# Kernel optimization log

Measured on AMD Instinct MI355X. Metric: run time of the kernel, lower is better.

## Reference

```python
import jax, jax.numpy as jnp
import numpy as np
import math

B, S, HID, NH = 2, 2048, 1024, 16
HD = HID // NH  # head_dim = 64
TEMPERATURE = 1.0


def setup_inputs() -> dict:
    key = jax.random.key(0)
    ks = jax.random.split(key, 6)
    w = lambda k: (jax.random.normal(k, (HID, HID), dtype=jnp.float32) * 0.02)
    return {
        "hidden_states": jax.random.normal(ks[0], (B, S, HID), dtype=jnp.float32),
        "attention_mask": jnp.ones((B, S), dtype=jnp.float32),
        "Wq": w(ks[1]), "bq": jnp.zeros((HID,), jnp.float32),
        "Wk": w(ks[2]), "bk": jnp.zeros((HID,), jnp.float32),
        "Wv": w(ks[3]), "bv": jnp.zeros((HID,), jnp.float32),
        "Wo": w(ks[4]), "bo": jnp.zeros((HID,), jnp.float32),
    }


def reference(hidden_states, attention_mask, Wq, bq, Wk, bk, Wv, bv, Wo, bo):
    b, s, hid = hidden_states.shape
    heads = lambda x: x.reshape(b, s, NH, HD).transpose(0, 2, 1, 3)  # [b,h,s,d]

    q = heads(hidden_states @ Wq.T + bq)
    k = heads(hidden_states @ Wk.T + bk)
    v = heads(hidden_states @ Wv.T + bv)

    # padding mask applied multiplicatively to k and v
    m = attention_mask[:, None, :, None]  # [b,1,s,1]
    k = k * m
    v = v * m

    # auxiliary Hopfield state: k^T @ v per head -> [b,h,d,d]
    state = jnp.einsum("bhsd,bhse->bhde", k, v)

    # energy / scores
    energy = jnp.einsum("bhqd,bhkd->bhqk", q, k) / (TEMPERATURE * math.sqrt(HD))
    causal = jnp.triu(jnp.ones((s, s), dtype=bool), k=1)  # True above diagonal
    energy = jnp.where(causal[None, None], -jnp.inf, energy)
    energy = jnp.where(attention_mask[:, None, None, :] == 0, -jnp.inf, energy)

    attn = jax.nn.softmax(energy, axis=-1)
    out = jnp.einsum("bhqk,bhkd->bhqd", attn, v)
    out = out.transpose(0, 2, 1, 3).reshape(b, s, hid)
    out = out @ Wo.T + bo
    return out, state
```

## Files before the change

kernel.cpp:

```cpp
#include <hip/hip_runtime.h>
#include <hip/hip_bf16.h>

#define B_ 2
#define S_ 2048
#define HID_ 1024
#define NH_ 16
#define HD_ 64
#define MTOK (B_*S_)
#define LDQKV 3072

typedef __attribute__((ext_vector_type(8))) __bf16 bf16x8;
typedef __attribute__((ext_vector_type(4))) __bf16 bf16x4;
typedef __attribute__((ext_vector_type(4))) float f32x4;

__device__ __forceinline__ void gl16(__bf16* lds, const __bf16* g) {
  __builtin_amdgcn_global_load_lds(
      (const __attribute__((address_space(1))) void*)g,
      (__attribute__((address_space(3))) void*)lds, 16, 0, 0);
}
__device__ __forceinline__ void gl4(float* lds, const float* g) {
  __builtin_amdgcn_global_load_lds(
      (const __attribute__((address_space(1))) void*)g,
      (__attribute__((address_space(3))) void*)lds, 4, 0, 0);
}

__global__ __launch_bounds__(256) void cast_all(
    const float* __restrict__ X,
    const float* __restrict__ Wq, const float* __restrict__ Wk,
    const float* __restrict__ Wv, const float* __restrict__ Wo,
    __bf16* __restrict__ Xb, __bf16* __restrict__ Wqkvb, __bf16* __restrict__ Wob)
{
  int i = blockIdx.x * 256 + threadIdx.x;
  const float* src; __bf16* dst; int j;
  if (i < (1 << 20))              { src = X;  dst = Xb;                 j = i; }
  else if (i < (1<<20)+(1<<18))   { src = Wq; dst = Wqkvb;              j = i - (1<<20); }
  else if (i < (1<<20)+(2<<18))   { src = Wk; dst = Wqkvb + (1<<20);    j = i - (1<<20) - (1<<18); }
  else if (i < (1<<20)+(3<<18))   { src = Wv; dst = Wqkvb + (2<<20);    j = i - (1<<20) - (2<<18); }
  else                            { src = Wo; dst = Wob;                j = i - (1<<20) - (3<<18); }
  float4 v = reinterpret_cast<const float4*>(src)[j];
  bf16x4 o;
  o[0] = (__bf16)v.x; o[1] = (__bf16)v.y; o[2] = (__bf16)v.z; o[3] = (__bf16)v.w;
  reinterpret_cast<bf16x4*>(dst)[j] = o;
}

__global__ __launch_bounds__(256) void gemm_qkv(
    const __bf16* __restrict__ A, const __bf16* __restrict__ W,
    const float* __restrict__ bq, const float* __restrict__ bk,
    const float* __restrict__ bv, const float* __restrict__ mask,
    __bf16* __restrict__ C)
{
  __shared__ __bf16 As[128 * 32];
  __shared__ __bf16 Bs[128 * 32];
  const int t = threadIdx.x;
  const int m0 = blockIdx.y * 128;
  const int n0 = blockIdx.x * 128;
  const int lane = t & 63;
  const int w = t >> 6;
  const int wr = (w >> 1) * 64;
  const int wc = (w & 1) * 64;
  const int fr = lane & 15;
  const int kg = lane >> 4;

  f32x4 acc[4][4];
  #pragma unroll
  for (int i = 0; i < 4; i++)
    #pragma unroll
    for (int j = 0; j < 4; j++) acc[i][j] = (f32x4)0.f;

  const int srow = w * 16 + (lane >> 2);
  const int scol = (lane & 3) * 8;
  const __bf16* ap0 = A + (size_t)(m0 + srow) * HID_ + scol;
  const __bf16* ap1 = A + (size_t)(m0 + 64 + srow) * HID_ + scol;
  const __bf16* wp0 = W + (size_t)(n0 + srow) * HID_ + scol;
  const __bf16* wp1 = W + (size_t)(n0 + 64 + srow) * HID_ + scol;

  for (int k0 = 0; k0 < HID_; k0 += 32) {
    __syncthreads();
    gl16(&As[w * 512], ap0 + k0);
    gl16(&As[2048 + w * 512], ap1 + k0);
    gl16(&Bs[w * 512], wp0 + k0);
    gl16(&Bs[2048 + w * 512], wp1 + k0);
    __syncthreads();
    bf16x8 af[4], bf[4];
    #pragma unroll
    for (int m = 0; m < 4; m++) af[m] = *(const bf16x8*)&As[(wr + m*16 + fr) * 32 + kg*8];
    #pragma unroll
    for (int n = 0; n < 4; n++) bf[n] = *(const bf16x8*)&Bs[(wc + n*16 + fr) * 32 + kg*8];
    #pragma unroll
    for (int m = 0; m < 4; m++)
      #pragma unroll
      for (int n = 0; n < 4; n++)
        acc[m][n] = __builtin_amdgcn_mfma_f32_16x16x32_bf16(af[m], bf[n], acc[m][n], 0, 0, 0);
  }

  const int region = n0 >> 10;
  const float* bias = region == 0 ? bq : (region == 1 ? bk : bv);
  const int nloc = n0 & 1023;

  #pragma unroll
  for (int m = 0; m < 4; m++) {
    #pragma unroll
    for (int r = 0; r < 4; r++) {
      int row = m0 + wr + m*16 + kg*4 + r;
      float rs = region ? mask[row] : 1.f;
      #pragma unroll
      for (int n = 0; n < 4; n++) {
        int c = wc + n*16 + fr;
        float v = (acc[m][n][r] + bias[nloc + c]) * rs;
        C[(size_t)row * LDQKV + n0 + c] = (__bf16)v;
      }
    }
  }
}

__global__ __launch_bounds__(256) void gemm_o(
    const __bf16* __restrict__ A, const __bf16* __restrict__ W,
    const float* __restrict__ bias, float* __restrict__ C)
{
  __shared__ __bf16 As[128 * 32];
  __shared__ __bf16 Bs[128 * 32];
  const int t = threadIdx.x;
  const int m0 = blockIdx.y * 128;
  const int n0 = blockIdx.x * 128;
  const int lane = t & 63;
  const int w = t >> 6;
  const int wr = (w >> 1) * 64;
  const int wc = (w & 1) * 64;
  const int fr = lane & 15;
  const int kg = lane >> 4;

  f32x4 acc[4][4];
  #pragma unroll
  for (int i = 0; i < 4; i++)
    #pragma unroll
    for (int j = 0; j < 4; j++) acc[i][j] = (f32x4)0.f;

  const int srow = w * 16 + (lane >> 2);
  const int scol = (lane & 3) * 8;
  const __bf16* ap0 = A + (size_t)(m0 + srow) * HID_ + scol;
  const __bf16* ap1 = A + (size_t)(m0 + 64 + srow) * HID_ + scol;
  const __bf16* wp0 = W + (size_t)(n0 + srow) * HID_ + scol;
  const __bf16* wp1 = W + (size_t)(n0 + 64 + srow) * HID_ + scol;

  for (int k0 = 0; k0 < HID_; k0 += 32) {
    __syncthreads();
    gl16(&As[w * 512], ap0 + k0);
    gl16(&As[2048 + w * 512], ap1 + k0);
    gl16(&Bs[w * 512], wp0 + k0);
    gl16(&Bs[2048 + w * 512], wp1 + k0);
    __syncthreads();
    bf16x8 af[4], bf[4];
    #pragma unroll
    for (int m = 0; m < 4; m++) af[m] = *(const bf16x8*)&As[(wr + m*16 + fr) * 32 + kg*8];
    #pragma unroll
    for (int n = 0; n < 4; n++) bf[n] = *(const bf16x8*)&Bs[(wc + n*16 + fr) * 32 + kg*8];
    #pragma unroll
    for (int m = 0; m < 4; m++)
      #pragma unroll
      for (int n = 0; n < 4; n++)
        acc[m][n] = __builtin_amdgcn_mfma_f32_16x16x32_bf16(af[m], bf[n], acc[m][n], 0, 0, 0);
  }

  #pragma unroll
  for (int m = 0; m < 4; m++) {
    #pragma unroll
    for (int r = 0; r < 4; r++) {
      int row = m0 + wr + m*16 + kg*4 + r;
      #pragma unroll
      for (int n = 0; n < 4; n++) {
        int col = n0 + wc + n*16 + fr;
        C[(size_t)row * HID_ + col] = acc[m][n][r] + bias[col];
      }
    }
  }
}

__global__ __launch_bounds__(256) void transpose_bf16(
    const __bf16* __restrict__ in, int ldin, __bf16* __restrict__ out)
{
  __shared__ __bf16 tile[64][68];
  const int tok0 = blockIdx.x * 64;
  const int f0 = blockIdx.y * 64;
  const int t = threadIdx.x;
  const int r = t >> 2;
  const int c0 = (t & 3) * 16;
  const __bf16* src = in + (size_t)(tok0 + r) * ldin + f0 + c0;
  *(bf16x8*)&tile[r][c0]     = *(const bf16x8*)src;
  *(bf16x8*)&tile[r][c0 + 8] = *(const bf16x8*)(src + 8);
  __syncthreads();
  bf16x8 o0, o1;
  #pragma unroll
  for (int j = 0; j < 8; j++) { o0[j] = tile[c0 + j][r]; o1[j] = tile[c0 + 8 + j][r]; }
  __bf16* dst = out + (size_t)(f0 + r) * MTOK + tok0 + c0;
  *(bf16x8*)dst = o0;
  *(bf16x8*)(dst + 8) = o1;
}

#define SCALE_LOG2E 0.18033688011112043f

__device__ __forceinline__ bf16x8 ld_swz(const __bf16* base, int row, int xb) {
  return *(const bf16x8*)((const char*)base + row * 128 + (xb ^ ((row & 7) << 4)));
}
__device__ __forceinline__ void st_swz16(__bf16* base, int row, int colbyte, __bf16 v) {
  *(__bf16*)((char*)base + row * 128 + (colbyte ^ ((row & 7) << 4))) = v;
}
__device__ __forceinline__ bf16x8 ld_swz256(const __bf16* base, int row, int xb) {
  return *(const bf16x8*)((const char*)base + row * 256 + (xb ^ ((row & 7) << 4)));
}

__global__ __launch_bounds__(512) void flash_mfma(
    const __bf16* __restrict__ Q, const __bf16* __restrict__ K,
    const __bf16* __restrict__ Vt, const float* __restrict__ mask,
    __bf16* __restrict__ O)
{
  __shared__ __bf16 Ks[2][64 * 64];
  __shared__ __bf16 Vs[2][64 * 64];
  __shared__ __bf16 Ps[8][16 * 64];
  __shared__ float mk[2][64];

  const int bh = blockIdx.x;
  const int qt = (int)(gridDim.y - 1) - (int)blockIdx.y;
  const int b = bh >> 4, h = bh & 15;
  const int t = threadIdx.x;
  const int w = t >> 6;
  const int lane = t & 63;
  const int fc = lane & 15;
  const int kg = lane >> 4;
  const int g4 = kg * 4;

  const int q0w = qt * 128 + w * 16;
  const size_t tokbase = (size_t)b * S_;

  const int rr = lane >> 3;
  const int cswz = ((lane & 7) ^ rr) * 8;
  const int ktmax = 2 * qt + 1;

  gl16(&Ks[0][w * 512], K + (tokbase + (size_t)(w * 8 + rr)) * LDQKV + h * HD_ + cswz);
  gl16(&Vs[0][w * 512], Vt + (size_t)(h * HD_ + w * 8 + rr) * MTOK + tokbase + cswz);
  gl4(&mk[0][0], mask + tokbase + lane);

  bf16x8 qa[2];
  {
    const __bf16* qp = Q + (tokbase + q0w + fc) * LDQKV + h * HD_;
    qa[0] = *(const bf16x8*)(qp + kg * 8);
    qa[1] = *(const bf16x8*)(qp + 32 + kg * 8);
  }

  bf16x8 ones;
  #pragma unroll
  for (int j = 0; j < 8; j++) ones[j] = (__bf16)1.f;

  f32x4 acc[4], accl;
  #pragma unroll
  for (int n = 0; n < 4; n++) acc[n] = (f32x4)0.f;
  accl = (f32x4)0.f;

  __bf16* pw = &Ps[w][0];

  for (int kt = 0; kt <= ktmax; ++kt) {
    const int cur = kt & 1;
    if (kt < ktmax) {
      const int nxt = cur ^ 1;
      gl16(&Ks[nxt][w * 512],
           K + (tokbase + (size_t)((kt + 1) * 64 + w * 8 + rr)) * LDQKV + h * HD_ + cswz);
      gl16(&Vs[nxt][w * 512],
           Vt + (size_t)(h * HD_ + w * 8 + rr) * MTOK + tokbase + (kt + 1) * 64 + cswz);
      gl4(&mk[nxt][0], mask + tokbase + (kt + 1) * 64 + lane);
      asm volatile("s_waitcnt vmcnt(3)" ::: "memory");
    } else {
      asm volatile("s_waitcnt vmcnt(0)" ::: "memory");
    }
    __builtin_amdgcn_sched_barrier(0);
    __builtin_amdgcn_s_barrier();

    if (kt * 64 <= q0w + 15) {
      const __bf16* ks = &Ks[cur][0];
      const __bf16* vs = &Vs[cur][0];
      f32x4 s[4];
      #pragma unroll
      for (int n = 0; n < 4; n++) s[n] = (f32x4)0.f;
      #pragma unroll
      for (int kd = 0; kd < 2; kd++)
        #pragma unroll
        for (int n = 0; n < 4; n++) {
          bf16x8 kf = ld_swz(ks, n * 16 + fc, kd * 64 + kg * 16);
          s[n] = __builtin_amdgcn_mfma_f32_16x16x32_bf16(qa[kd], kf, s[n], 0, 0, 0);
        }

      bool okm[4];
      #pragma unroll
      for (int n = 0; n < 4; n++) okm[n] = (mk[cur][n * 16 + fc] != 0.f);

      const bool fullt = (kt * 64 + 63 <= q0w);
      if (fullt) {
        #pragma unroll
        for (int r = 0; r < 4; r++)
          #pragma unroll
          for (int n = 0; n < 4; n++) {
            float p = okm[n] ? exp2f(s[n][r] * SCALE_LOG2E) : 0.f;
            st_swz16(pw, g4 + r, (n * 16 + fc) * 2, (__bf16)p);
          }
      } else {
        #pragma unroll
        for (int r = 0; r < 4; r++) {
          const int qg = q0w + g4 + r;
          #pragma unroll
          for (int n = 0; n < 4; n++) {
            bool ok = okm[n] && (kt * 64 + n * 16 + fc <= qg);
            float p = ok ? exp2f(s[n][r] * SCALE_LOG2E) : 0.f;
            st_swz16(pw, g4 + r, (n * 16 + fc) * 2, (__bf16)p);
          }
        }
      }

      #pragma unroll
      for (int kc = 0; kc < 2; kc++) {
        bf16x8 pf = ld_swz(pw, fc, kc * 64 + kg * 16);
        accl = __builtin_amdgcn_mfma_f32_16x16x32_bf16(pf, ones, accl, 0, 0, 0);
        #pragma unroll
        for (int n = 0; n < 4; n++) {
          bf16x8 vf = ld_swz(vs, n * 16 + fc, kc * 64 + kg * 16);
          acc[n] = __builtin_amdgcn_mfma_f32_16x16x32_bf16(pf, vf, acc[n], 0, 0, 0);
        }
      }
    }
    __builtin_amdgcn_s_barrier();
  }

  #pragma unroll
  for (int r = 0; r < 4; r++) {
    float inv = accl[r] > 0.f ? 1.f / accl[r] : 0.f;
    __bf16* op = O + (tokbase + q0w + g4 + r) * HID_ + h * HD_;
    #pragma unroll
    for (int n = 0; n < 4; n++)
      op[n * 16 + fc] = (__bf16)(acc[n][r] * inv);
  }
}

__global__ __launch_bounds__(256) void state_mfma(
    const __bf16* __restrict__ Kt, const __bf16* __restrict__ Vt,
    float* __restrict__ part)
{
  __shared__ __bf16 Kl[64 * 128];
  __shared__ __bf16 Vl[64 * 128];
  const int bh = blockIdx.x, sc = blockIdx.y;
  const int b = bh >> 4, h = bh & 15;
  const int t = threadIdx.x;
  const int w = t >> 6;
  const int lane = t & 63;
  const int fc = lane & 15;
  const int kg = lane >> 4;
  const size_t colbase = (size_t)b * S_ + sc * 128;
  const int rloc = lane >> 4;
  const int cb = (lane & 15) * 16;

  #pragma unroll
  for (int c = 0; c < 4; c++) {
    int row = w * 16 + c * 4 + rloc;
    int scol = (cb ^ ((row & 7) << 4)) >> 1;
    gl16(&Kl[(w * 16 + c * 4) * 128], Kt + (size_t)(h * HD_ + row) * MTOK + colbase + scol);
    gl16(&Vl[(w * 16 + c * 4) * 128], Vt + (size_t)(h * HD_ + row) * MTOK + colbase + scol);
  }
  __syncthreads();

  f32x4 acc[4];
  #pragma unroll
  for (int n = 0; n < 4; n++) acc[n] = (f32x4)0.f;
  #pragma unroll
  for (int ks = 0; ks < 4; ks++) {
    bf16x8 af = ld_swz256(Kl, w * 16 + fc, ks * 64 + kg * 16);
    #pragma unroll
    for (int n = 0; n < 4; n++) {
      bf16x8 bfr = ld_swz256(Vl, n * 16 + fc, ks * 64 + kg * 16);
      acc[n] = __builtin_amdgcn_mfma_f32_16x16x32_bf16(af, bfr, acc[n], 0, 0, 0);
    }
  }

  float* dst = part + (((size_t)bh * 16 + sc) << 12);
  #pragma unroll
  for (int n = 0; n < 4; n++)
    #pragma unroll
    for (int r = 0; r < 4; r++)
      dst[(w * 16 + kg * 4 + r) * 64 + n * 16 + fc] = acc[n][r];
}

__global__ __launch_bounds__(256) void state_reduce(
    const float* __restrict__ part, float* __restrict__ out)
{
  int i = blockIdx.x * 256 + threadIdx.x;
  int bh = i >> 12, de = i & 4095;
  float s = 0.f;
  #pragma unroll
  for (int sc = 0; sc < 16; sc++) s += part[(((size_t)bh * 16 + sc) << 12) + de];
  out[i] = s;
}

extern "C" void kernel_launch(void* const* d_in, const int* in_sizes, int n_in,
                              void* d_out, int out_size, void* d_ws, size_t ws_size,
                              hipStream_t stream)
{
  const float* hs   = (const float*)d_in[0];
  const float* mask = (const float*)d_in[1];
  const float* Wq   = (const float*)d_in[2];
  const float* bq   = (const float*)d_in[3];
  const float* Wk   = (const float*)d_in[4];
  const float* bk   = (const float*)d_in[5];
  const float* Wv   = (const float*)d_in[6];
  const float* bv   = (const float*)d_in[7];
  const float* Wo   = (const float*)d_in[8];
  const float* bo   = (const float*)d_in[9];
  float* out = (float*)d_out;

  char* ws = (char*)d_ws;
  __bf16* Wqkvb = (__bf16*)(ws);
  __bf16* Wob   = (__bf16*)(ws + (6u  << 20));
  __bf16* Xb    = (__bf16*)(ws + (8u  << 20));
  __bf16* QKV   = (__bf16*)(ws + (16u << 20));
  __bf16* Ob    = (__bf16*)(ws + (40u << 20));
  float*  part  = (float*)(ws + (48u << 20));

  cast_all<<<8192, 256, 0, stream>>>(hs, Wq, Wk, Wv, Wo, Xb, Wqkvb, Wob);

  gemm_qkv<<<dim3(LDQKV / 128, MTOK / 128), 256, 0, stream>>>(
      Xb, Wqkvb, bq, bk, bv, mask, QKV);

  __bf16* Vtg = Xb;
  transpose_bf16<<<dim3(MTOK / 64, HID_ / 64), 256, 0, stream>>>(QKV + 2048, LDQKV, Vtg);

  flash_mfma<<<dim3(B_ * NH_, S_ / 128), 512, 0, stream>>>(
      QKV, QKV + 1024, Vtg, mask, Ob);

  gemm_o<<<dim3(HID_ / 128, MTOK / 128), 256, 0, stream>>>(Ob, Wob, bo, out);

  __bf16* Ktg = Wqkvb;
  transpose_bf16<<<dim3(MTOK / 64, HID_ / 64), 256, 0, stream>>>(QKV + 1024, LDQKV, Ktg);

  state_mfma<<<dim3(B_ * NH_, 16), 256, 0, stream>>>(Ktg, Vtg, part);
  state_reduce<<<512, 256, 0, stream>>>(part, out + (size_t)MTOK * HID_);
}
```

Baseline: 144.1 us.

## Pair causal query tiles per block and merge K/V transposes into one launch

The flash attention kernel now has each block handle two query tiles, y and 15-y. The causal work per block is therefore balanced, and each K/V tile loaded into shared memory serves both query tiles, while the grid is halved to 8 tiles per head. The separate K and V transpose kernels are merged into a single launch with a z dimension. Buffers are remapped so the state partials reuse the Ob region after gemm_o. The cost is more registers per thread (two accumulator sets), which may lower occupancy, and fewer blocks overall.

```diff
diff --git a/kernel.cpp b/kernel.cpp
--- a/kernel.cpp
+++ b/kernel.cpp
@@ -175,16 +175,19 @@
   }
 }
 
-__global__ __launch_bounds__(256) void transpose_bf16(
-    const __bf16* __restrict__ in, int ldin, __bf16* __restrict__ out)
+__global__ __launch_bounds__(256) void transpose_kv(
+    const __bf16* __restrict__ Kin, const __bf16* __restrict__ Vin,
+    __bf16* __restrict__ Kt, __bf16* __restrict__ Vt)
 {
   __shared__ __bf16 tile[64][68];
   const int tok0 = blockIdx.x * 64;
   const int f0 = blockIdx.y * 64;
+  const __bf16* in = blockIdx.z ? Vin : Kin;
+  __bf16* out = blockIdx.z ? Vt : Kt;
   const int t = threadIdx.x;
   const int r = t >> 2;
   const int c0 = (t & 3) * 16;
-  const __bf16* src = in + (size_t)(tok0 + r) * ldin + f0 + c0;
+  const __bf16* src = in + (size_t)(tok0 + r) * LDQKV + f0 + c0;
   *(bf16x8*)&tile[r][c0]     = *(const bf16x8*)src;
   *(bf16x8*)&tile[r][c0 + 8] = *(const bf16x8*)(src + 8);
   __syncthreads();
@@ -208,6 +211,58 @@
   return *(const bf16x8*)((const char*)base + row * 256 + (xb ^ ((row & 7) << 4)));
 }
 
+__device__ __forceinline__ void attn_tile(
+    const __bf16* __restrict__ ks, const __bf16* __restrict__ vs,
+    const bool (&okm)[4], __bf16* __restrict__ pw,
+    const bf16x8 (&qa)[2], f32x4 (&acc)[4], f32x4& accl,
+    const bf16x8 ones, int q0w, int kt, int fc, int kg)
+{
+  f32x4 s[4];
+  #pragma unroll
+  for (int n = 0; n < 4; n++) s[n] = (f32x4)0.f;
+  #pragma unroll
+  for (int kd = 0; kd < 2; kd++)
+    #pragma unroll
+    for (int n = 0; n < 4; n++) {
+      bf16x8 kf = ld_swz(ks, n * 16 + fc, kd * 64 + kg * 16);
+      s[n] = __builtin_amdgcn_mfma_f32_16x16x32_bf16(qa[kd], kf, s[n], 0, 0, 0);
+    }
+
+  const int g4 = kg * 4;
+  const bool fullt = (kt * 64 + 63 <= q0w);
+  if (fullt) {
+    #pragma unroll
+    for (int r = 0; r < 4; r++)
+      #pragma unroll
+      for (int n = 0; n < 4; n++) {
+        float p = okm[n] ? exp2f(s[n][r] * SCALE_LOG2E) : 0.f;
+        st_swz16(pw, g4 + r, (n * 16 + fc) * 2, (__bf16)p);
+      }
+  } else {
+    #pragma unroll
+    for (int r = 0; r < 4; r++) {
+      const int qg = q0w + g4 + r;
+      #pragma unroll
+      for (int n = 0; n < 4; n++) {
+        bool ok = okm[n] && (kt * 64 + n * 16 + fc <= qg);
+        float p = ok ? exp2f(s[n][r] * SCALE_LOG2E) : 0.f;
+        st_swz16(pw, g4 + r, (n * 16 + fc) * 2, (__bf16)p);
+      }
+    }
+  }
+
+  #pragma unroll
+  for (int kc = 0; kc < 2; kc++) {
+    bf16x8 pf = ld_swz(pw, fc, kc * 64 + kg * 16);
+    accl = __builtin_amdgcn_mfma_f32_16x16x32_bf16(pf, ones, accl, 0, 0, 0);
+    #pragma unroll
+    for (int n = 0; n < 4; n++) {
+      bf16x8 vf = ld_swz(vs, n * 16 + fc, kc * 64 + kg * 16);
+      acc[n] = __builtin_amdgcn_mfma_f32_16x16x32_bf16(pf, vf, acc[n], 0, 0, 0);
+    }
+  }
+}
+
 __global__ __launch_bounds__(512) void flash_mfma(
     const __bf16* __restrict__ Q, const __bf16* __restrict__ K,
     const __bf16* __restrict__ Vt, const float* __restrict__ mask,
@@ -215,11 +270,12 @@
 {
   __shared__ __bf16 Ks[2][64 * 64];
   __shared__ __bf16 Vs[2][64 * 64];
-  __shared__ __bf16 Ps[8][16 * 64];
+  __shared__ __bf16 Ps[8][2][16 * 64];
   __shared__ float mk[2][64];
 
   const int bh = blockIdx.x;
-  const int qt = (int)(gridDim.y - 1) - (int)blockIdx.y;
+  const int y = blockIdx.y;
+  const int qtA = y, qtB = 15 - y;
   const int b = bh >> 4, h = bh & 15;
   const int t = threadIdx.x;
   const int w = t >> 6;
@@ -228,34 +284,39 @@
   const int kg = lane >> 4;
   const int g4 = kg * 4;
 
-  const int q0w = qt * 128 + w * 16;
+  const int q0A = qtA * 128 + w * 16;
+  const int q0B = qtB * 128 + w * 16;
   const size_t tokbase = (size_t)b * S_;
 
   const int rr = lane >> 3;
   const int cswz = ((lane & 7) ^ rr) * 8;
-  const int ktmax = 2 * qt + 1;
+  const int ktmax = 2 * qtB + 1;
 
   gl16(&Ks[0][w * 512], K + (tokbase + (size_t)(w * 8 + rr)) * LDQKV + h * HD_ + cswz);
   gl16(&Vs[0][w * 512], Vt + (size_t)(h * HD_ + w * 8 + rr) * MTOK + tokbase + cswz);
   gl4(&mk[0][0], mask + tokbase + lane);
 
-  bf16x8 qa[2];
+  bf16x8 qaA[2], qaB[2];
   {
-    const __bf16* qp = Q + (tokbase + q0w + fc) * LDQKV + h * HD_;
-    qa[0] = *(const bf16x8*)(qp + kg * 8);
-    qa[1] = *(const bf16x8*)(qp + 32 + kg * 8);
+    const __bf16* qp = Q + (tokbase + q0A + fc) * LDQKV + h * HD_;
+    qaA[0] = *(const bf16x8*)(qp + kg * 8);
+    qaA[1] = *(const bf16x8*)(qp + 32 + kg * 8);
+    const __bf16* qp2 = Q + (tokbase + q0B + fc) * LDQKV + h * HD_;
+    qaB[0] = *(const bf16x8*)(qp2 + kg * 8);
+    qaB[1] = *(const bf16x8*)(qp2 + 32 + kg * 8);
   }
 
   bf16x8 ones;
   #pragma unroll
   for (int j = 0; j < 8; j++) ones[j] = (__bf16)1.f;
 
-  f32x4 acc[4], accl;
-  #pragma unroll
-  for (int n = 0; n < 4; n++) acc[n] = (f32x4)0.f;
-  accl = (f32x4)0.f;
-
-  __bf16* pw = &Ps[w][0];
+  f32x4 accA[4], acclA, accB[4], acclB;
+  #pragma unroll
+  for (int n = 0; n < 4; n++) { accA[n] = (f32x4)0.f; accB[n] = (f32x4)0.f; }
+  acclA = (f32x4)0.f; acclB = (f32x4)0.f;
+
+  __bf16* pwA = &Ps[w][0][0];
+  __bf16* pwB = &Ps[w][1][0];
 
   for (int kt = 0; kt <= ktmax; ++kt) {
     const int cur = kt & 1;
@@ -273,67 +334,28 @@
     __builtin_amdgcn_sched_barrier(0);
     __builtin_amdgcn_s_barrier();
 
-    if (kt * 64 <= q0w + 15) {
-      const __bf16* ks = &Ks[cur][0];
-      const __bf16* vs = &Vs[cur][0];
-      f32x4 s[4];
-      #pragma unroll
-      for (int n = 0; n < 4; n++) s[n] = (f32x4)0.f;
-      #pragma unroll
-      for (int kd = 0; kd < 2; kd++)
-        #pragma unroll
-        for (int n = 0; n < 4; n++) {
-          bf16x8 kf = ld_swz(ks, n * 16 + fc, kd * 64 + kg * 16);
-          s[n] = __builtin_amdgcn_mfma_f32_16x16x32_bf16(qa[kd], kf, s[n], 0, 0, 0);
-        }
-
-      bool okm[4];
-      #pragma unroll
-      for (int n = 0; n < 4; n++) okm[n] = (mk[cur][n * 16 + fc] != 0.f);
-
-      const bool fullt = (kt * 64 + 63 <= q0w);
-      if (fullt) {
-        #pragma unroll
-        for (int r = 0; r < 4; r++)
-          #pragma unroll
-          for (int n = 0; n < 4; n++) {
-            float p = okm[n] ? exp2f(s[n][r] * SCALE_LOG2E) : 0.f;
-            st_swz16(pw, g4 + r, (n * 16 + fc) * 2, (__bf16)p);
-          }
-      } else {
-        #pragma unroll
-        for (int r = 0; r < 4; r++) {
-          const int qg = q0w + g4 + r;
-          #pragma unroll
-          for (int n = 0; n < 4; n++) {
-            bool ok = okm[n] && (kt * 64 + n * 16 + fc <= qg);
-            float p = ok ? exp2f(s[n][r] * SCALE_LOG2E) : 0.f;
-            st_swz16(pw, g4 + r, (n * 16 + fc) * 2, (__bf16)p);
-          }
-        }
-      }
-
-      #pragma unroll
-      for (int kc = 0; kc < 2; kc++) {
-        bf16x8 pf = ld_swz(pw, fc, kc * 64 + kg * 16);
-        accl = __builtin_amdgcn_mfma_f32_16x16x32_bf16(pf, ones, accl, 0, 0, 0);
-        #pragma unroll
-        for (int n = 0; n < 4; n++) {
-          bf16x8 vf = ld_swz(vs, n * 16 + fc, kc * 64 + kg * 16);
-          acc[n] = __builtin_amdgcn_mfma_f32_16x16x32_bf16(pf, vf, acc[n], 0, 0, 0);
-        }
-      }
-    }
+    bool okm[4];
+    #pragma unroll
+    for (int n = 0; n < 4; n++) okm[n] = (mk[cur][n * 16 + fc] != 0.f);
+
+    if (kt * 64 <= q0A + 15)
+      attn_tile(&Ks[cur][0], &Vs[cur][0], okm, pwA, qaA, accA, acclA, ones, q0A, kt, fc, kg);
+    attn_tile(&Ks[cur][0], &Vs[cur][0], okm, pwB, qaB, accB, acclB, ones, q0B, kt, fc, kg);
+
     __builtin_amdgcn_s_barrier();
   }
 
   #pragma unroll
   for (int r = 0; r < 4; r++) {
-    float inv = accl[r] > 0.f ? 1.f / accl[r] : 0.f;
-    __bf16* op = O + (tokbase + q0w + g4 + r) * HID_ + h * HD_;
-    #pragma unroll
-    for (int n = 0; n < 4; n++)
-      op[n * 16 + fc] = (__bf16)(acc[n][r] * inv);
+    float invA = acclA[r] > 0.f ? 1.f / acclA[r] : 0.f;
+    float invB = acclB[r] > 0.f ? 1.f / acclB[r] : 0.f;
+    __bf16* opA = O + (tokbase + q0A + g4 + r) * HID_ + h * HD_;
+    __bf16* opB = O + (tokbase + q0B + g4 + r) * HID_ + h * HD_;
+    #pragma unroll
+    for (int n = 0; n < 4; n++) {
+      opA[n * 16 + fc] = (__bf16)(accA[n][r] * invA);
+      opB[n * 16 + fc] = (__bf16)(accB[n][r] * invB);
+    }
   }
 }
 
@@ -417,7 +439,7 @@
   __bf16* Xb    = (__bf16*)(ws + (8u  << 20));
   __bf16* QKV   = (__bf16*)(ws + (16u << 20));
   __bf16* Ob    = (__bf16*)(ws + (40u << 20));
-  float*  part  = (float*)(ws + (48u << 20));
+  __bf16* Ktg   = (__bf16*)(ws + (48u << 20));
 
   cast_all<<<8192, 256, 0, stream>>>(hs, Wq, Wk, Wv, Wo, Xb, Wqkvb, Wob);
 
@@ -425,16 +447,15 @@
       Xb, Wqkvb, bq, bk, bv, mask, QKV);
 
   __bf16* Vtg = Xb;
-  transpose_bf16<<<dim3(MTOK / 64, HID_ / 64), 256, 0, stream>>>(QKV + 2048, LDQKV, Vtg);
-
-  flash_mfma<<<dim3(B_ * NH_, S_ / 128), 512, 0, stream>>>(
+  transpose_kv<<<dim3(MTOK / 64, HID_ / 64, 2), 256, 0, stream>>>(
+      QKV + 1024, QKV + 2048, Ktg, Vtg);
+
+  flash_mfma<<<dim3(B_ * NH_, 8), 512, 0, stream>>>(
       QKV, QKV + 1024, Vtg, mask, Ob);
 
   gemm_o<<<dim3(HID_ / 128, MTOK / 128), 256, 0, stream>>>(Ob, Wob, bo, out);
 
-  __bf16* Ktg = Wqkvb;
-  transpose_bf16<<<dim3(MTOK / 64, HID_ / 64), 256, 0, stream>>>(QKV + 1024, LDQKV, Ktg);
-
+  float* part = (float*)Ob;
   state_mfma<<<dim3(B_ * NH_, 16), 256, 0, stream>>>(Ktg, Vtg, part);
   state_reduce<<<512, 256, 0, stream>>>(part, out + (size_t)MTOK * HID_);
 }
```

Result: slower. 147.9 us (+2.6%).
